# Kernel optimization log

Hardware: AMD Instinct MI355X
Metric: run time of the kernel (lower is better)

The kernel has to match this reference:

```python
import jax, jax.numpy as jnp
import numpy as np

NUM_HEADS = 16

def _apply_rope(x, cos, sin):
    # x: (B, H, T, D); cos/sin: (T, D//2)
    B, H, T, D = x.shape
    xr = x.reshape(B, H, T, D // 2, 2)
    x0, x1 = xr[..., 0], xr[..., 1]
    c = cos[None, None, :, :]
    s = sin[None, None, :, :]
    out = jnp.stack([x0 * c - x1 * s, x0 * s + x1 * c], axis=-1)
    return out.reshape(B, H, T, D)


def setup_inputs() -> dict:
    key = jax.random.key(0)
    k1, k2, k3 = jax.random.split(key, 3)
    B, T, C = 2, 2048, 1024
    D = C // NUM_HEADS
    x = jax.random.normal(k1, (B, T, C), dtype=jnp.float32)
    qkv_w = jax.random.normal(k2, (3 * C, C), dtype=jnp.float32) * (C ** -0.5)
    proj_w = jax.random.normal(k3, (C, C), dtype=jnp.float32) * (C ** -0.5)
    # standard RoPE frequency table (theta = 10000)
    inv_freq = 1.0 / (10000.0 ** (jnp.arange(0, D, 2, dtype=jnp.float32) / D))  # (D/2,)
    angles = jnp.arange(T, dtype=jnp.float32)[:, None] * inv_freq[None, :]      # (T, D/2)
    return {
        "x": x,
        "freqs_cos": jnp.cos(angles),
        "freqs_sin": jnp.sin(angles),
        "qkv_w": qkv_w,
        "proj_w": proj_w,
    }


def reference(x, freqs_cos, freqs_sin, qkv_w, proj_w):
    B, T, C = x.shape
    H = NUM_HEADS
    D = C // H
    qkv = x @ qkv_w.T                                  # (B, T, 3C)
    q, k, v = jnp.split(qkv, 3, axis=-1)
    q = q.reshape(B, T, H, D).transpose(0, 2, 1, 3)    # (B, H, T, D)
    k = k.reshape(B, T, H, D).transpose(0, 2, 1, 3)
    v = v.reshape(B, T, H, D).transpose(0, 2, 1, 3)
    q = _apply_rope(q, freqs_cos, freqs_sin)
    k = _apply_rope(k, freqs_cos, freqs_sin)
    scale = 1.0 / jnp.sqrt(jnp.asarray(D, dtype=x.dtype))
    scores = jnp.einsum('bhqd,bhkd->bhqk', q, k) * scale
    causal = jnp.tril(jnp.ones((T, T), dtype=bool))
    scores = jnp.where(causal[None, None], scores, jnp.finfo(scores.dtype).min)
    attn = jax.nn.softmax(scores, axis=-1)
    out = jnp.einsum('bhqk,bhkd->bhqd', attn, v)       # (B, H, T, D)
    out = out.transpose(0, 2, 1, 3).reshape(B, T, C)
    return out @ proj_w.T
```

## Files before the change

### kernel.cpp

```cpp
#include <hip/hip_runtime.h>
#include <stdint.h>

#define DI __device__ __forceinline__

typedef unsigned short u16;
typedef __bf16 bf16x8 __attribute__((ext_vector_type(8)));
typedef unsigned short u16x8 __attribute__((ext_vector_type(8)));
typedef unsigned short u16x4 __attribute__((ext_vector_type(4)));
typedef float f32x4 __attribute__((ext_vector_type(4)));

DI u16 f2bf(float f) { __bf16 h = (__bf16)f; return __builtin_bit_cast(u16, h); }
DI float bf2f(u16 u) { return (float)__builtin_bit_cast(__bf16, u); }

DI bf16x8 ld8(const u16* p) { return __builtin_bit_cast(bf16x8, *(const u16x8*)p); }

DI f32x4 mfma16(bf16x8 a, bf16x8 b, f32x4 c) {
  return __builtin_amdgcn_mfma_f32_16x16x32_bf16(a, b, c, 0, 0, 0);
}

DI void async16(const u16* g, u16* l) {
  __builtin_amdgcn_global_load_lds((const __attribute__((address_space(1))) void*)g,
                                   (__attribute__((address_space(3))) void*)l, 16, 0, 0);
}

__global__ __launch_bounds__(256) void cast_bf16_k(const float* __restrict__ in,
                                                   u16* __restrict__ out) {
  const int i = blockIdx.x * 256 + threadIdx.x;
  const float4 v = ((const float4*)in)[i];
  u16x4 o = {f2bf(v.x), f2bf(v.y), f2bf(v.z), f2bf(v.w)};
  ((u16x4*)out)[i] = o;
}

template <int OUT_BF16>
__global__ __launch_bounds__(256) void gemm_bt(const u16* __restrict__ A,
                                               const u16* __restrict__ W,
                                               void* __restrict__ outp,
                                               int M, int N, int K) {
  __shared__ u16 sA[2 * 4096];
  __shared__ u16 sB[2 * 4096];
  const int tid = threadIdx.x;
  const int w = tid >> 6, L = tid & 63;
  const int lo = L & 15, quad = L >> 4;
  const int nb = N >> 7;
  const int bm = blockIdx.x / nb, bn = blockIdx.x - bm * nb;
  const int m0 = bm << 7, n0 = bn << 7;
  const int wm = (w >> 1) << 6, wn = (w & 1) << 6;

  f32x4 acc[4][4];
#pragma unroll
  for (int i = 0; i < 4; ++i)
#pragma unroll
    for (int j = 0; j < 4; ++j) acc[i][j] = 0.f;

  const int r0 = tid >> 2, s0 = tid & 3;
  const int c0 = s0 ^ ((r0 >> 1) & 3);
  const int r1 = r0 + 64;
  const int c1 = s0 ^ ((r1 >> 1) & 3);
  const size_t aRow0 = (size_t)(m0 + r0) * K, aRow1 = (size_t)(m0 + r1) * K;
  const size_t bRow0 = (size_t)(n0 + r0) * K, bRow1 = (size_t)(n0 + r1) * K;

  int raf[4], rbf[4];
#pragma unroll
  for (int mt = 0; mt < 4; ++mt) {
    int r = wm + mt * 16 + lo;
    raf[mt] = r * 32 + ((quad ^ ((r >> 1) & 3)) << 3);
    r = wn + mt * 16 + lo;
    rbf[mt] = r * 32 + ((quad ^ ((r >> 1) & 3)) << 3);
  }

  auto stage = [&](int kb, int buf) {
    const int bo = buf << 12;
    async16(A + aRow0 + kb + c0 * 8, &sA[bo + tid * 8]);
    async16(A + aRow1 + kb + c1 * 8, &sA[bo + (tid + 256) * 8]);
    async16(W + bRow0 + kb + c0 * 8, &sB[bo + tid * 8]);
    async16(W + bRow1 + kb + c1 * 8, &sB[bo + (tid + 256) * 8]);
  };

  const int kIters = K >> 5;
  stage(0, 0);
  for (int kt = 0; kt < kIters; ++kt) {
    __syncthreads();
    if (kt + 1 < kIters) stage((kt + 1) << 5, (kt + 1) & 1);
    const int bo = (kt & 1) << 12;
    bf16x8 af[4], bfr[4];
#pragma unroll
    for (int mt = 0; mt < 4; ++mt) af[mt] = ld8(&sA[bo + raf[mt]]);
#pragma unroll
    for (int nt = 0; nt < 4; ++nt) bfr[nt] = ld8(&sB[bo + rbf[nt]]);
#pragma unroll
    for (int mt = 0; mt < 4; ++mt)
#pragma unroll
      for (int nt = 0; nt < 4; ++nt)
        acc[mt][nt] = mfma16(af[mt], bfr[nt], acc[mt][nt]);
  }

#pragma unroll
  for (int mt = 0; mt < 4; ++mt) {
    const int m = m0 + wm + mt * 16 + quad * 4;
#pragma unroll
    for (int nt = 0; nt < 4; ++nt) {
      const int n = n0 + wn + nt * 16 + lo;
#pragma unroll
      for (int r = 0; r < 4; ++r) {
        const size_t off = (size_t)(m + r) * N + n;
        if (OUT_BF16)
          ((u16*)outp)[off] = f2bf(acc[mt][nt][r]);
        else
          ((float*)outp)[off] = acc[mt][nt][r];
      }
    }
  }
}

#define QSCALE 0.18033688011112f
__global__ __launch_bounds__(256) void rope_k(const u16* __restrict__ qkv,
                                              const float* __restrict__ cosb,
                                              const float* __restrict__ sinb,
                                              u16* __restrict__ qo, u16* __restrict__ ko) {
  const int idx = blockIdx.x * 256 + threadIdx.x;
  const int i = idx & 31;
  const int t = (idx >> 5) & 2047;
  const int h = (idx >> 16) & 15;
  const int b = idx >> 20;
  const size_t src = ((size_t)(b * 2048 + t)) * 3072 + h * 64 + 2 * i;
  const float q0v = bf2f(qkv[src]), q1v = bf2f(qkv[src + 1]);
  const float k0v = bf2f(qkv[src + 1024]), k1v = bf2f(qkv[src + 1025]);
  const float c = cosb[t * 32 + i], s = sinb[t * 32 + i];
  const size_t dst = ((size_t)((b * 16 + h) * 2048 + t)) * 64 + 2 * i;
  qo[dst] = f2bf((q0v * c - q1v * s) * QSCALE);
  qo[dst + 1] = f2bf((q0v * s + q1v * c) * QSCALE);
  ko[dst] = f2bf(k0v * c - k1v * s);
  ko[dst + 1] = f2bf(k0v * s + k1v * c);
}

__global__ __launch_bounds__(256) void vt_k(const u16* __restrict__ qkv,
                                            u16* __restrict__ vt) {
  __shared__ u16 sT[64 * 64];
  const int tid = threadIdx.x;
  const int bh = blockIdx.x & 31;
  const int t0 = (blockIdx.x >> 5) << 6;
  const int b = bh >> 4, h = bh & 15;
#pragma unroll
  for (int it = 0; it < 2; ++it) {
    const int id = tid + it * 256;
    const int tr = id >> 3, s = id & 7, c = s ^ (tr & 7);
    async16(qkv + (size_t)(b * 2048 + t0 + tr) * 3072 + 2048 + h * 64 + c * 8, &sT[id * 8]);
  }
  __syncthreads();
#pragma unroll
  for (int it = 0; it < 2; ++it) {
    const int id = tid + it * 256;
    const int d = id >> 3, ct = id & 7;
    u16x8 o;
#pragma unroll
    for (int j = 0; j < 8; ++j) {
      const int t = ct * 8 + j;
      o[j] = sT[t * 64 + (((d >> 3) ^ (t & 7)) << 3) + (d & 7)];
    }
    *(u16x8*)(vt + ((size_t)bh * 64 + d) * 2048 + t0 + ct * 8) = o;
  }
}

__global__ __launch_bounds__(256) void fattn(const u16* __restrict__ qs,
                                             const u16* __restrict__ ks,
                                             const u16* __restrict__ vt,
                                             u16* __restrict__ aout) {
  __shared__ u16 sK[2 * 4096];
  __shared__ u16 sVt[2 * 4096];
  __shared__ u16 sP[4][16 * 64];
  const int tid = threadIdx.x;
  const int w = tid >> 6, L = tid & 63;
  const int lo = L & 15, quad = L >> 4;
  const int bh = blockIdx.x & 31;
  const int qi = 31 - (blockIdx.x >> 5);
  const size_t hoff = (size_t)bh * (2048 * 64);
  const int q0 = qi << 6;
  const int wq = q0 + w * 16;
  u16* sPw = sP[w];

  auto stage = [&](int kv0, int buf) {
    const int bo = buf << 12;
#pragma unroll
    for (int it = 0; it < 2; ++it) {
      const int id = tid + it * 256;
      const int kv = id >> 3, s = id & 7, c = s ^ (kv & 7);
      async16(ks + hoff + (size_t)(kv0 + kv) * 64 + c * 8, &sK[bo + id * 8]);
    }
#pragma unroll
    for (int it = 0; it < 2; ++it) {
      const int id = tid + it * 256;
      const int d = id >> 3, s = id & 7, c = s ^ (d & 7);
      async16(vt + hoff + (size_t)d * 2048 + kv0 + c * 8, &sVt[bo + id * 8]);
    }
  };

  bf16x8 qb[2];
#pragma unroll
  for (int kd = 0; kd < 2; ++kd)
    qb[kd] = ld8(qs + hoff + (size_t)(wq + lo) * 64 + kd * 32 + quad * 8);

  float m_s = -3.0e38f, l_s = 0.f;
  f32x4 ot[4];
#pragma unroll
  for (int mt = 0; mt < 4; ++mt) ot[mt] = 0.f;

  const int ntiles = qi + 1;
  stage(0, 0);
  for (int kt = 0; kt < ntiles; ++kt) {
    __syncthreads();
    if (kt + 1 < ntiles) stage((kt + 1) << 6, (kt + 1) & 1);
    const int bo = (kt & 1) << 12;
    const int kv0 = kt << 6;

    f32x4 st[4];
#pragma unroll
    for (int mt = 0; mt < 4; ++mt) st[mt] = 0.f;
#pragma unroll
    for (int mt = 0; mt < 4; ++mt) {
      const int kv = mt * 16 + lo;
#pragma unroll
      for (int kd = 0; kd < 2; ++kd) {
        const int c = kd * 4 + quad;
        bf16x8 ka = ld8(&sK[bo + kv * 64 + ((c ^ (kv & 7)) << 3)]);
        st[mt] = mfma16(ka, qb[kd], st[mt]);
      }
    }
    if (kt == qi) {
      const int qg = wq + lo;
#pragma unroll
      for (int mt = 0; mt < 4; ++mt)
#pragma unroll
        for (int r = 0; r < 4; ++r) {
          const int kvg = kv0 + mt * 16 + quad * 4 + r;
          if (kvg > qg) st[mt][r] = -3.0e38f;
        }
    }
    float mx = -3.0e38f;
#pragma unroll
    for (int mt = 0; mt < 4; ++mt)
#pragma unroll
      for (int r = 0; r < 4; ++r) mx = fmaxf(mx, st[mt][r]);
    mx = fmaxf(mx, __shfl_xor(mx, 16));
    mx = fmaxf(mx, __shfl_xor(mx, 32));
    const float mnew = fmaxf(m_s, mx);
    const float alpha = __builtin_amdgcn_exp2f(m_s - mnew);
    float rs = 0.f;
#pragma unroll
    for (int mt = 0; mt < 4; ++mt)
#pragma unroll
      for (int r = 0; r < 4; ++r) {
        const float p = __builtin_amdgcn_exp2f(st[mt][r] - mnew);
        st[mt][r] = p;
        rs += p;
      }
    rs += __shfl_xor(rs, 16);
    rs += __shfl_xor(rs, 32);
    l_s = l_s * alpha + rs;
    m_s = mnew;
#pragma unroll
    for (int mt = 0; mt < 4; ++mt) {
      u16x4 pk = {f2bf(st[mt][0]), f2bf(st[mt][1]), f2bf(st[mt][2]), f2bf(st[mt][3])};
      const int c2 = 2 * mt + (quad >> 1);
      *(u16x4*)&sPw[lo * 64 + ((c2 ^ (lo & 7)) << 3) + (quad & 1) * 4] = pk;
    }
#pragma unroll
    for (int mt = 0; mt < 4; ++mt)
#pragma unroll
      for (int r = 0; r < 4; ++r) ot[mt][r] *= alpha;
    asm volatile("s_waitcnt lgkmcnt(0)" ::: "memory");
    bf16x8 pbf[2];
#pragma unroll
    for (int kh = 0; kh < 2; ++kh) {
      const int c = kh * 4 + quad;
      pbf[kh] = ld8(&sPw[lo * 64 + ((c ^ (lo & 7)) << 3)]);
    }
#pragma unroll
    for (int mt = 0; mt < 4; ++mt) {
      const int d = mt * 16 + lo;
#pragma unroll
      for (int kh = 0; kh < 2; ++kh) {
        const int c = kh * 4 + quad;
        bf16x8 va = ld8(&sVt[bo + d * 64 + ((c ^ (d & 7)) << 3)]);
        ot[mt] = mfma16(va, pbf[kh], ot[mt]);
      }
    }
  }

  const float iv = 1.f / l_s;
#pragma unroll
  for (int mt = 0; mt < 4; ++mt) {
    u16x4 ok = {f2bf(ot[mt][0] * iv), f2bf(ot[mt][1] * iv), f2bf(ot[mt][2] * iv),
                f2bf(ot[mt][3] * iv)};
    const int c2 = 2 * mt + (quad >> 1);
    *(u16x4*)&sPw[lo * 64 + ((c2 ^ (lo & 7)) << 3) + (quad & 1) * 4] = ok;
  }
  asm volatile("s_waitcnt lgkmcnt(0)" ::: "memory");
  const int b = bh >> 4, h = bh & 15;
#pragma unroll
  for (int rr = 0; rr < 2; ++rr) {
    const int q = rr * 8 + (L >> 3);
    const int cd = L & 7;
    u16x8 o8 = *(const u16x8*)&sPw[q * 64 + ((cd ^ (q & 7)) << 3)];
    const int t = wq + q;
    *(u16x8*)(aout + ((size_t)(b * 2048 + t)) * 1024 + h * 64 + cd * 8) = o8;
  }
}

extern "C" void kernel_launch(void* const* d_in, const int* in_sizes, int n_in,
                              void* d_out, int out_size, void* d_ws, size_t ws_size,
                              hipStream_t stream) {
  const float* x = (const float*)d_in[0];
  const float* fcos = (const float*)d_in[1];
  const float* fsin = (const float*)d_in[2];
  const float* qkvw = (const float*)d_in[3];
  const float* projw = (const float*)d_in[4];
  float* out = (float*)d_out;

  char* ws = (char*)d_ws;
  u16* x_bf = (u16*)(ws);
  u16* qkvw_bf = (u16*)(ws + (8u << 20));
  u16* projw_bf = (u16*)(ws + (14u << 20));
  u16* qkv_bf = (u16*)(ws + (16u << 20));
  u16* q_bf = (u16*)(ws + (40u << 20));
  u16* k_bf = (u16*)(ws + (48u << 20));
  u16* vt = (u16*)(ws + (56u << 20));
  u16* attn_bf = (u16*)(ws + (64u << 20));

  cast_bf16_k<<<4096, 256, 0, stream>>>(x, x_bf);
  cast_bf16_k<<<3072, 256, 0, stream>>>(qkvw, qkvw_bf);
  cast_bf16_k<<<1024, 256, 0, stream>>>(projw, projw_bf);
  gemm_bt<1><<<768, 256, 0, stream>>>(x_bf, qkvw_bf, (void*)qkv_bf, 4096, 3072, 1024);
  rope_k<<<8192, 256, 0, stream>>>(qkv_bf, fcos, fsin, q_bf, k_bf);
  vt_k<<<1024, 256, 0, stream>>>(qkv_bf, vt);
  fattn<<<1024, 256, 0, stream>>>(q_bf, k_bf, vt, attn_bf);
  gemm_bt<0><<<256, 256, 0, stream>>>(attn_bf, projw_bf, (void*)out, 4096, 1024, 1024);
}
```

Before: 198.5 us.

## Split attention KV range across two blocks and merge, fuse small kernels

Flash attention now splits each query tile's causal KV range into two halves handled by separate blocks. Each block writes an unnormalized partial output plus its running max and sum, and a new merge kernel combines the two halves. This doubles the grid to improve load balance and occupancy on the causal triangle, at the cost of extra partial-output traffic and one more launch. Separately, the three cast kernels are fused into one, rope and V-transpose are fused into one launch, and address arithmetic is hoisted into incrementing pointers and precomputed LDS offsets in the GEMM and attention loops.

```diff
diff --git a/kernel.cpp b/kernel.cpp
--- a/kernel.cpp
+++ b/kernel.cpp
@@ -23,12 +23,26 @@
                                    (__attribute__((address_space(3))) void*)l, 16, 0, 0);
 }
 
-__global__ __launch_bounds__(256) void cast_bf16_k(const float* __restrict__ in,
-                                                   u16* __restrict__ out) {
-  const int i = blockIdx.x * 256 + threadIdx.x;
-  const float4 v = ((const float4*)in)[i];
+__global__ __launch_bounds__(256) void cast_all(const float* __restrict__ x,
+                                                const float* __restrict__ qw,
+                                                const float* __restrict__ pw,
+                                                u16* __restrict__ xb, u16* __restrict__ qwb,
+                                                u16* __restrict__ pwb) {
+  const int bi = blockIdx.x;
+  const float* src;
+  u16* dst;
+  int off;
+  if (bi < 4096) {
+    src = x; dst = xb; off = bi;
+  } else if (bi < 7168) {
+    src = qw; dst = qwb; off = bi - 4096;
+  } else {
+    src = pw; dst = pwb; off = bi - 7168;
+  }
+  const int i = off * 256 + threadIdx.x;
+  const float4 v = ((const float4*)src)[i];
   u16x4 o = {f2bf(v.x), f2bf(v.y), f2bf(v.z), f2bf(v.w)};
-  ((u16x4*)out)[i] = o;
+  ((u16x4*)dst)[i] = o;
 }
 
 template <int OUT_BF16>
@@ -56,8 +70,14 @@
   const int c0 = s0 ^ ((r0 >> 1) & 3);
   const int r1 = r0 + 64;
   const int c1 = s0 ^ ((r1 >> 1) & 3);
-  const size_t aRow0 = (size_t)(m0 + r0) * K, aRow1 = (size_t)(m0 + r1) * K;
-  const size_t bRow0 = (size_t)(n0 + r0) * K, bRow1 = (size_t)(n0 + r1) * K;
+  const u16* aP0 = A + (size_t)(m0 + r0) * K + c0 * 8;
+  const u16* aP1 = A + (size_t)(m0 + r1) * K + c1 * 8;
+  const u16* bP0 = W + (size_t)(n0 + r0) * K + c0 * 8;
+  const u16* bP1 = W + (size_t)(n0 + r1) * K + c1 * 8;
+  u16* ldA0 = &sA[tid * 8];
+  u16* ldA1 = &sA[(tid + 256) * 8];
+  u16* ldB0 = &sB[tid * 8];
+  u16* ldB1 = &sB[(tid + 256) * 8];
 
   int raf[4], rbf[4];
 #pragma unroll
@@ -68,19 +88,20 @@
     rbf[mt] = r * 32 + ((quad ^ ((r >> 1) & 3)) << 3);
   }
 
-  auto stage = [&](int kb, int buf) {
+  auto stage = [&](int buf) {
     const int bo = buf << 12;
-    async16(A + aRow0 + kb + c0 * 8, &sA[bo + tid * 8]);
-    async16(A + aRow1 + kb + c1 * 8, &sA[bo + (tid + 256) * 8]);
-    async16(W + bRow0 + kb + c0 * 8, &sB[bo + tid * 8]);
-    async16(W + bRow1 + kb + c1 * 8, &sB[bo + (tid + 256) * 8]);
+    async16(aP0, ldA0 + bo);
+    async16(aP1, ldA1 + bo);
+    async16(bP0, ldB0 + bo);
+    async16(bP1, ldB1 + bo);
+    aP0 += 32; aP1 += 32; bP0 += 32; bP1 += 32;
   };
 
   const int kIters = K >> 5;
-  stage(0, 0);
+  stage(0);
   for (int kt = 0; kt < kIters; ++kt) {
     __syncthreads();
-    if (kt + 1 < kIters) stage((kt + 1) << 5, (kt + 1) & 1);
+    if (kt + 1 < kIters) stage((kt + 1) & 1);
     const int bo = (kt & 1) << 12;
     bf16x8 af[4], bfr[4];
 #pragma unroll
@@ -113,86 +134,114 @@
 }
 
 #define QSCALE 0.18033688011112f
-__global__ __launch_bounds__(256) void rope_k(const u16* __restrict__ qkv,
-                                              const float* __restrict__ cosb,
-                                              const float* __restrict__ sinb,
-                                              u16* __restrict__ qo, u16* __restrict__ ko) {
-  const int idx = blockIdx.x * 256 + threadIdx.x;
-  const int i = idx & 31;
-  const int t = (idx >> 5) & 2047;
-  const int h = (idx >> 16) & 15;
-  const int b = idx >> 20;
-  const size_t src = ((size_t)(b * 2048 + t)) * 3072 + h * 64 + 2 * i;
-  const float q0v = bf2f(qkv[src]), q1v = bf2f(qkv[src + 1]);
-  const float k0v = bf2f(qkv[src + 1024]), k1v = bf2f(qkv[src + 1025]);
-  const float c = cosb[t * 32 + i], s = sinb[t * 32 + i];
-  const size_t dst = ((size_t)((b * 16 + h) * 2048 + t)) * 64 + 2 * i;
-  qo[dst] = f2bf((q0v * c - q1v * s) * QSCALE);
-  qo[dst + 1] = f2bf((q0v * s + q1v * c) * QSCALE);
-  ko[dst] = f2bf(k0v * c - k1v * s);
-  ko[dst + 1] = f2bf(k0v * s + k1v * c);
-}
-
-__global__ __launch_bounds__(256) void vt_k(const u16* __restrict__ qkv,
-                                            u16* __restrict__ vt) {
+__global__ __launch_bounds__(256) void ropevt_k(const u16* __restrict__ qkv,
+                                                const float* __restrict__ cosb,
+                                                const float* __restrict__ sinb,
+                                                u16* __restrict__ qo, u16* __restrict__ ko,
+                                                u16* __restrict__ vto) {
   __shared__ u16 sT[64 * 64];
   const int tid = threadIdx.x;
-  const int bh = blockIdx.x & 31;
-  const int t0 = (blockIdx.x >> 5) << 6;
-  const int b = bh >> 4, h = bh & 15;
-#pragma unroll
-  for (int it = 0; it < 2; ++it) {
-    const int id = tid + it * 256;
-    const int tr = id >> 3, s = id & 7, c = s ^ (tr & 7);
-    async16(qkv + (size_t)(b * 2048 + t0 + tr) * 3072 + 2048 + h * 64 + c * 8, &sT[id * 8]);
-  }
-  __syncthreads();
-#pragma unroll
-  for (int it = 0; it < 2; ++it) {
-    const int id = tid + it * 256;
-    const int d = id >> 3, ct = id & 7;
-    u16x8 o;
-#pragma unroll
-    for (int j = 0; j < 8; ++j) {
-      const int t = ct * 8 + j;
-      o[j] = sT[t * 64 + (((d >> 3) ^ (t & 7)) << 3) + (d & 7)];
-    }
-    *(u16x8*)(vt + ((size_t)bh * 64 + d) * 2048 + t0 + ct * 8) = o;
-  }
-}
-
-__global__ __launch_bounds__(256) void fattn(const u16* __restrict__ qs,
-                                             const u16* __restrict__ ks,
-                                             const u16* __restrict__ vt,
-                                             u16* __restrict__ aout) {
+  if (blockIdx.x < 8192) {
+    const int idx = blockIdx.x * 256 + tid;
+    const int i = idx & 31;
+    const int t = (idx >> 5) & 2047;
+    const int h = (idx >> 16) & 15;
+    const int b = idx >> 20;
+    const size_t src = ((size_t)(b * 2048 + t)) * 3072 + h * 64 + 2 * i;
+    const float q0v = bf2f(qkv[src]), q1v = bf2f(qkv[src + 1]);
+    const float k0v = bf2f(qkv[src + 1024]), k1v = bf2f(qkv[src + 1025]);
+    const float c = cosb[t * 32 + i], s = sinb[t * 32 + i];
+    const size_t dst = ((size_t)((b * 16 + h) * 2048 + t)) * 64 + 2 * i;
+    qo[dst] = f2bf((q0v * c - q1v * s) * QSCALE);
+    qo[dst + 1] = f2bf((q0v * s + q1v * c) * QSCALE);
+    ko[dst] = f2bf(k0v * c - k1v * s);
+    ko[dst + 1] = f2bf(k0v * s + k1v * c);
+  } else {
+    const int bi = blockIdx.x - 8192;
+    const int bh = bi & 31;
+    const int t0 = (bi >> 5) << 6;
+    const int b = bh >> 4, h = bh & 15;
+#pragma unroll
+    for (int it = 0; it < 2; ++it) {
+      const int id = tid + it * 256;
+      const int tr = id >> 3, s = id & 7, c = s ^ (tr & 7);
+      async16(qkv + (size_t)(b * 2048 + t0 + tr) * 3072 + 2048 + h * 64 + c * 8, &sT[id * 8]);
+    }
+    __syncthreads();
+#pragma unroll
+    for (int it = 0; it < 2; ++it) {
+      const int id = tid + it * 256;
+      const int d = id >> 3, ct = id & 7;
+      u16x8 o;
+#pragma unroll
+      for (int j = 0; j < 8; ++j) {
+        const int t = ct * 8 + j;
+        o[j] = sT[t * 64 + (((d >> 3) ^ (t & 7)) << 3) + (d & 7)];
+      }
+      *(u16x8*)(vto + ((size_t)bh * 64 + d) * 2048 + t0 + ct * 8) = o;
+    }
+  }
+}
+
+__global__ __launch_bounds__(256) void fattn_part(const u16* __restrict__ qs,
+                                                  const u16* __restrict__ ks,
+                                                  const u16* __restrict__ vtb,
+                                                  u16* __restrict__ opart,
+                                                  float2* __restrict__ ml) {
   __shared__ u16 sK[2 * 4096];
   __shared__ u16 sVt[2 * 4096];
   __shared__ u16 sP[4][16 * 64];
   const int tid = threadIdx.x;
   const int w = tid >> 6, L = tid & 63;
   const int lo = L & 15, quad = L >> 4;
-  const int bh = blockIdx.x & 31;
-  const int qi = 31 - (blockIdx.x >> 5);
+  const int raw = blockIdx.x;
+  const int part = raw & 1;
+  const int bh = (raw >> 1) & 31;
+  const int qi = 31 - (raw >> 6);
+  const int n = qi + 1;
+  const int h0 = (n + 1) >> 1;
+  const int tk0 = part ? h0 : 0;
+  const int tk1 = part ? n : h0;
   const size_t hoff = (size_t)bh * (2048 * 64);
-  const int q0 = qi << 6;
-  const int wq = q0 + w * 16;
+  const int wq = (qi << 6) + w * 16;
   u16* sPw = sP[w];
 
-  auto stage = [&](int kv0, int buf) {
+  const int kvA = tid >> 3, cA = (tid & 7) ^ (kvA & 7);
+  const int idB = tid + 256;
+  const int kvB = idB >> 3, cB = (idB & 7) ^ (kvB & 7);
+  const u16* kP0 = ks + hoff + (size_t)(tk0 * 64 + kvA) * 64 + cA * 8;
+  const u16* kP1 = ks + hoff + (size_t)(tk0 * 64 + kvB) * 64 + cB * 8;
+  const u16* vP0 = vtb + hoff + (size_t)kvA * 2048 + tk0 * 64 + cA * 8;
+  const u16* vP1 = vtb + hoff + (size_t)kvB * 2048 + tk0 * 64 + cB * 8;
+  u16* ldK0 = &sK[tid * 8];
+  u16* ldK1 = &sK[idB * 8];
+  u16* ldV0 = &sVt[tid * 8];
+  u16* ldV1 = &sVt[idB * 8];
+
+  auto stage = [&](int buf) {
     const int bo = buf << 12;
-#pragma unroll
-    for (int it = 0; it < 2; ++it) {
-      const int id = tid + it * 256;
-      const int kv = id >> 3, s = id & 7, c = s ^ (kv & 7);
-      async16(ks + hoff + (size_t)(kv0 + kv) * 64 + c * 8, &sK[bo + id * 8]);
-    }
-#pragma unroll
-    for (int it = 0; it < 2; ++it) {
-      const int id = tid + it * 256;
-      const int d = id >> 3, s = id & 7, c = s ^ (d & 7);
-      async16(vt + hoff + (size_t)d * 2048 + kv0 + c * 8, &sVt[bo + id * 8]);
-    }
+    async16(kP0, ldK0 + bo);
+    async16(kP1, ldK1 + bo);
+    async16(vP0, ldV0 + bo);
+    async16(vP1, ldV1 + bo);
+    kP0 += 4096; kP1 += 4096; vP0 += 64; vP1 += 64;
   };
+
+  int kaOff[4][2], vaOff[4][2], pOff[2], pwOff[4];
+#pragma unroll
+  for (int mt = 0; mt < 4; ++mt) {
+    const int kv = mt * 16 + lo;
+#pragma unroll
+    for (int kd = 0; kd < 2; ++kd) {
+      const int c = kd * 4 + quad;
+      kaOff[mt][kd] = kv * 64 + ((c ^ (kv & 7)) << 3);
+      vaOff[mt][kd] = kaOff[mt][kd];
+    }
+    const int c2 = 2 * mt + (quad >> 1);
+    pwOff[mt] = lo * 64 + ((c2 ^ (lo & 7)) << 3) + (quad & 1) * 4;
+  }
+#pragma unroll
+  for (int kh = 0; kh < 2; ++kh) pOff[kh] = lo * 64 + (((kh * 4 + quad) ^ (lo & 7)) << 3);
 
   bf16x8 qb[2];
 #pragma unroll
@@ -204,29 +253,26 @@
 #pragma unroll
   for (int mt = 0; mt < 4; ++mt) ot[mt] = 0.f;
 
-  const int ntiles = qi + 1;
-  stage(0, 0);
-  for (int kt = 0; kt < ntiles; ++kt) {
+  const int ntk = tk1 - tk0;
+  if (ntk > 0) stage(0);
+  for (int it2 = 0; it2 < ntk; ++it2) {
     __syncthreads();
-    if (kt + 1 < ntiles) stage((kt + 1) << 6, (kt + 1) & 1);
-    const int bo = (kt & 1) << 12;
-    const int kv0 = kt << 6;
+    if (it2 + 1 < ntk) stage((it2 + 1) & 1);
+    const int bo = (it2 & 1) << 12;
+    const int kt = tk0 + it2;
 
     f32x4 st[4];
 #pragma unroll
     for (int mt = 0; mt < 4; ++mt) st[mt] = 0.f;
 #pragma unroll
-    for (int mt = 0; mt < 4; ++mt) {
-      const int kv = mt * 16 + lo;
-#pragma unroll
-      for (int kd = 0; kd < 2; ++kd) {
-        const int c = kd * 4 + quad;
-        bf16x8 ka = ld8(&sK[bo + kv * 64 + ((c ^ (kv & 7)) << 3)]);
-        st[mt] = mfma16(ka, qb[kd], st[mt]);
-      }
-    }
+    for (int mt = 0; mt < 4; ++mt)
+#pragma unroll
+      for (int kd = 0; kd < 2; ++kd)
+        st[mt] = mfma16(ld8(&sK[bo + kaOff[mt][kd]]), qb[kd], st[mt]);
+
     if (kt == qi) {
       const int qg = wq + lo;
+      const int kv0 = kt << 6;
 #pragma unroll
       for (int mt = 0; mt < 4; ++mt)
 #pragma unroll
@@ -260,8 +306,7 @@
 #pragma unroll
     for (int mt = 0; mt < 4; ++mt) {
       u16x4 pk = {f2bf(st[mt][0]), f2bf(st[mt][1]), f2bf(st[mt][2]), f2bf(st[mt][3])};
-      const int c2 = 2 * mt + (quad >> 1);
-      *(u16x4*)&sPw[lo * 64 + ((c2 ^ (lo & 7)) << 3) + (quad & 1) * 4] = pk;
+      *(u16x4*)&sPw[pwOff[mt]] = pk;
     }
 #pragma unroll
     for (int mt = 0; mt < 4; ++mt)
@@ -270,39 +315,55 @@
     asm volatile("s_waitcnt lgkmcnt(0)" ::: "memory");
     bf16x8 pbf[2];
 #pragma unroll
-    for (int kh = 0; kh < 2; ++kh) {
-      const int c = kh * 4 + quad;
-      pbf[kh] = ld8(&sPw[lo * 64 + ((c ^ (lo & 7)) << 3)]);
-    }
-#pragma unroll
-    for (int mt = 0; mt < 4; ++mt) {
-      const int d = mt * 16 + lo;
-#pragma unroll
-      for (int kh = 0; kh < 2; ++kh) {
-        const int c = kh * 4 + quad;
-        bf16x8 va = ld8(&sVt[bo + d * 64 + ((c ^ (d & 7)) << 3)]);
-        ot[mt] = mfma16(va, pbf[kh], ot[mt]);
-      }
-    }
-  }
-
-  const float iv = 1.f / l_s;
+    for (int kh = 0; kh < 2; ++kh) pbf[kh] = ld8(&sPw[pOff[kh]]);
+#pragma unroll
+    for (int mt = 0; mt < 4; ++mt)
+#pragma unroll
+      for (int kh = 0; kh < 2; ++kh)
+        ot[mt] = mfma16(ld8(&sVt[bo + vaOff[mt][kh]]), pbf[kh], ot[mt]);
+  }
+
+  const int pq = bh * 32 + qi;
+  u16* obase = opart + (size_t)(part * 1024 + pq) * 4096 + (size_t)(w * 16 + lo) * 64;
 #pragma unroll
   for (int mt = 0; mt < 4; ++mt) {
-    u16x4 ok = {f2bf(ot[mt][0] * iv), f2bf(ot[mt][1] * iv), f2bf(ot[mt][2] * iv),
-                f2bf(ot[mt][3] * iv)};
-    const int c2 = 2 * mt + (quad >> 1);
-    *(u16x4*)&sPw[lo * 64 + ((c2 ^ (lo & 7)) << 3) + (quad & 1) * 4] = ok;
-  }
-  asm volatile("s_waitcnt lgkmcnt(0)" ::: "memory");
+    const int d0 = mt * 16 + quad * 4;
+    u16x4 ok = {f2bf(ot[mt][0]), f2bf(ot[mt][1]), f2bf(ot[mt][2]), f2bf(ot[mt][3])};
+    *(u16x4*)&obase[d0] = ok;
+  }
+  if (quad == 0) {
+    float2 v;
+    v.x = m_s;
+    v.y = l_s;
+    ml[(size_t)(part * 1024 + pq) * 64 + w * 16 + lo] = v;
+  }
+}
+
+__global__ __launch_bounds__(256) void fattn_merge(const u16* __restrict__ opart,
+                                                   const float2* __restrict__ ml,
+                                                   u16* __restrict__ aout) {
+  const int pq = blockIdx.x;
+  const int bh = pq >> 5, qi = pq & 31;
   const int b = bh >> 4, h = bh & 15;
-#pragma unroll
-  for (int rr = 0; rr < 2; ++rr) {
-    const int q = rr * 8 + (L >> 3);
-    const int cd = L & 7;
-    u16x8 o8 = *(const u16x8*)&sPw[q * 64 + ((cd ^ (q & 7)) << 3)];
-    const int t = wq + q;
-    *(u16x8*)(aout + ((size_t)(b * 2048 + t)) * 1024 + h * 64 + cd * 8) = o8;
+  const int tid = threadIdx.x;
+#pragma unroll
+  for (int it = 0; it < 2; ++it) {
+    const int idx = tid + it * 256;
+    const int q = idx >> 3, d0 = (idx & 7) * 8;
+    const float2 ml0 = ml[(size_t)pq * 64 + q];
+    const float2 ml1 = ml[(size_t)(1024 + pq) * 64 + q];
+    const float ms = fmaxf(ml0.x, ml1.x);
+    float w0 = __builtin_amdgcn_exp2f(ml0.x - ms);
+    float w1 = __builtin_amdgcn_exp2f(ml1.x - ms);
+    const float inv = 1.f / (w0 * ml0.y + w1 * ml1.y);
+    w0 *= inv;
+    w1 *= inv;
+    const u16x8 o0 = *(const u16x8*)&opart[(size_t)pq * 4096 + q * 64 + d0];
+    const u16x8 o1 = *(const u16x8*)&opart[(size_t)(1024 + pq) * 4096 + q * 64 + d0];
+    u16x8 o;
+#pragma unroll
+    for (int j = 0; j < 8; ++j) o[j] = f2bf(w0 * bf2f(o0[j]) + w1 * bf2f(o1[j]));
+    *(u16x8*)&aout[((size_t)(b * 2048 + qi * 64 + q)) * 1024 + h * 64 + d0] = o;
   }
 }
 
@@ -325,13 +386,13 @@
   u16* k_bf = (u16*)(ws + (48u << 20));
   u16* vt = (u16*)(ws + (56u << 20));
   u16* attn_bf = (u16*)(ws + (64u << 20));
-
-  cast_bf16_k<<<4096, 256, 0, stream>>>(x, x_bf);
-  cast_bf16_k<<<3072, 256, 0, stream>>>(qkvw, qkvw_bf);
-  cast_bf16_k<<<1024, 256, 0, stream>>>(projw, projw_bf);
+  u16* opart = (u16*)(ws + (16u << 20));
+  float2* mlb = (float2*)(ws + (32u << 20));
+
+  cast_all<<<8192, 256, 0, stream>>>(x, qkvw, projw, x_bf, qkvw_bf, projw_bf);
   gemm_bt<1><<<768, 256, 0, stream>>>(x_bf, qkvw_bf, (void*)qkv_bf, 4096, 3072, 1024);
-  rope_k<<<8192, 256, 0, stream>>>(qkv_bf, fcos, fsin, q_bf, k_bf);
-  vt_k<<<1024, 256, 0, stream>>>(qkv_bf, vt);
-  fattn<<<1024, 256, 0, stream>>>(q_bf, k_bf, vt, attn_bf);
+  ropevt_k<<<9216, 256, 0, stream>>>(qkv_bf, fcos, fsin, q_bf, k_bf, vt);
+  fattn_part<<<2048, 256, 0, stream>>>(q_bf, k_bf, vt, opart, mlb);
+  fattn_merge<<<1024, 256, 0, stream>>>(opart, mlb, attn_bf);
   gemm_bt<0><<<256, 256, 0, stream>>>(attn_bf, projw_bf, (void*)out, 4096, 1024, 1024);
 }
```

After: 195.3 us. About the same (-1.6%).
